# Performance work log

Hardware: AMD Instinct MI355X
Metric: run time of the kernel (lower is better)

Reference implementation:

```python
import jax, jax.numpy as jnp
import numpy as np

IN_FEATURES = 4096
OUT_FEATURES = 11008
BATCH = 16


def setup_inputs() -> dict:
    key = jax.random.key(0)
    k_x, k_w, k_s, k_b = jax.random.split(key, 4)
    x = jax.random.normal(k_x, (BATCH, IN_FEATURES), dtype=jnp.float32)
    # symmetric int8 weights stored as int32 for jax portability (values in [-127, 127])
    weight_int8 = jax.random.randint(k_w, (OUT_FEATURES, IN_FEATURES), -127, 128, dtype=jnp.int32)
    # per-output-channel scales, small positive values typical of int8 quantization
    weight_scale = jax.random.uniform(k_s, (OUT_FEATURES,), dtype=jnp.float32, minval=0.005, maxval=0.02)
    bias = jax.random.normal(k_b, (OUT_FEATURES,), dtype=jnp.float32)
    return {"x": x, "weight_int8": weight_int8, "weight_scale": weight_scale, "bias": bias}


def reference(x, weight_int8, weight_scale, bias):
    # Dequantize: w_dq[o, i] = int8[o, i] * scale[o]  -> fp32 [OUT, IN]
    w_dq = weight_int8.astype(x.dtype) * weight_scale[:, None]
    # F.linear: y = x @ w_dq.T + bias  -> [BATCH, OUT]
    return jnp.einsum("bi,oi->bo", x, w_dq) + bias
```

## Files before the change

### kernel.cpp

```cpp
#include <hip/hip_runtime.h>

#define IN_F   4096
#define OUT_F  11008
#define BATCH  16
#define BLOCK  256
#define SPLITK 8
#define KCHUNK (IN_F / SPLITK)
#define XPAD   8
#define XSTRIDE (KCHUNK + XPAD)
#define NSTEP  (KCHUNK / 32)

typedef short s16x8 __attribute__((ext_vector_type(8)));
typedef float f32x4 __attribute__((ext_vector_type(4)));
typedef int   i32x4 __attribute__((ext_vector_type(4)));

__global__ __launch_bounds__(BLOCK) void init_out_kernel(
    const float* __restrict__ bias, float* __restrict__ out)
{
    int idx = blockIdx.x * BLOCK + threadIdx.x;
    if (idx < BATCH * OUT_F) {
        int o = idx % OUT_F;
        out[idx] = bias[o];
    }
}

__device__ __forceinline__ unsigned short bf16_trunc_bits(float f) {
    return (unsigned short)(__float_as_uint(f) >> 16);
}

__global__ __launch_bounds__(BLOCK) void qlin_kernel(
    const float* __restrict__ x,
    const int*   __restrict__ w,
    const float* __restrict__ scale,
    float* __restrict__ out)
{
    __shared__ alignas(16) unsigned short xhi[BATCH * XSTRIDE];
    __shared__ alignas(16) unsigned short xlo[BATCH * XSTRIDE];

    const int tid  = threadIdx.x;
    const int lane = tid & 63;
    const int wv   = tid >> 6;
    const int n    = lane & 15;
    const int quad = lane >> 4;
    const int o0   = blockIdx.x * 64 + wv * 16;
    const int kb   = blockIdx.y * KCHUNK;

    const float4* __restrict__ xg = (const float4*)x;
    #pragma unroll
    for (int j = 0; j < (BATCH * KCHUNK / 4) / BLOCK; ++j) {
        int f  = tid + j * BLOCK;
        int b  = f >> 7;
        int kc = f & 127;
        float4 v = xg[(size_t)b * (IN_F / 4) + (kb >> 2) + kc];
        ushort4 h, l;
        {
            unsigned u;
            u = __float_as_uint(v.x); h.x = u >> 16;
            l.x = bf16_trunc_bits(v.x - __uint_as_float(u & 0xFFFF0000u));
            u = __float_as_uint(v.y); h.y = u >> 16;
            l.y = bf16_trunc_bits(v.y - __uint_as_float(u & 0xFFFF0000u));
            u = __float_as_uint(v.z); h.z = u >> 16;
            l.z = bf16_trunc_bits(v.z - __uint_as_float(u & 0xFFFF0000u));
            u = __float_as_uint(v.w); h.w = u >> 16;
            l.w = bf16_trunc_bits(v.w - __uint_as_float(u & 0xFFFF0000u));
        }
        *(ushort4*)&xhi[b * XSTRIDE + kc * 4] = h;
        *(ushort4*)&xlo[b * XSTRIDE + kc * 4] = l;
    }
    __syncthreads();

    const int* __restrict__ wrow = w + (size_t)(o0 + n) * IN_F + kb + quad * 8;
    i32x4 wa[2], wb[2];
    wa[0] = *(const i32x4*)(wrow);
    wb[0] = *(const i32x4*)(wrow + 4);

    f32x4 acc = {0.f, 0.f, 0.f, 0.f};

    #pragma unroll
    for (int s = 0; s < NSTEP; ++s) {
        const int cur = s & 1, nxt = cur ^ 1;
        if (s + 1 < NSTEP) {
            wa[nxt] = *(const i32x4*)(wrow + (s + 1) * 32);
            wb[nxt] = *(const i32x4*)(wrow + (s + 1) * 32 + 4);
        }

        s16x8 bfrag;
        #pragma unroll
        for (int e = 0; e < 4; ++e) {
            bfrag[e]     = (short)bf16_trunc_bits((float)wa[cur][e]);
            bfrag[4 + e] = (short)bf16_trunc_bits((float)wb[cur][e]);
        }

        const int xoff = n * XSTRIDE + s * 32 + quad * 8;
        s16x8 ah = *(const s16x8*)&xhi[xoff];
        s16x8 al = *(const s16x8*)&xlo[xoff];

        acc = __builtin_amdgcn_mfma_f32_16x16x32_bf16(ah, bfrag, acc, 0, 0, 0);
        acc = __builtin_amdgcn_mfma_f32_16x16x32_bf16(al, bfrag, acc, 0, 0, 0);
    }

    const int   o  = o0 + n;
    const float sc = scale[o];
    #pragma unroll
    for (int r = 0; r < 4; ++r) {
        const int b = quad * 4 + r;
        atomicAdd(&out[(size_t)b * OUT_F + o], acc[r] * sc);
    }
}

extern "C" void kernel_launch(void* const* d_in, const int* in_sizes, int n_in,
                              void* d_out, int out_size, void* d_ws, size_t ws_size,
                              hipStream_t stream) {
    const float* x     = (const float*)d_in[0];
    const int*   w     = (const int*)d_in[1];
    const float* scale = (const float*)d_in[2];
    const float* bias  = (const float*)d_in[3];
    float* out = (float*)d_out;

    init_out_kernel<<<(BATCH * OUT_F + BLOCK - 1) / BLOCK, BLOCK, 0, stream>>>(bias, out);

    dim3 grid(OUT_F / 64, SPLITK);
    qlin_kernel<<<grid, dim3(BLOCK), 0, stream>>>(x, w, scale, out);
}
```

Measured before the change: 261.8 us.

## Precompute bf16 hi/lo split of x in prep kernel, stream weights nontemporally

Moves the fp32-to-bf16 hi/lo splitting of x out of every qlin block and into a single prep kernel that also writes the bias init. The results go to workspace buffers. The main kernel now reads the x fragments straight from global memory with double-buffered prefetch, replacing the shared-memory staging and the __syncthreads barrier. Weight loads use nontemporal hints so the one-pass weight stream is less likely to evict x from cache. The x split also switches from truncation to round-to-nearest-even. The cost is one workspace round trip and x loads that now depend on L2/L1 hits instead of LDS.

```diff
diff --git a/kernel.cpp b/kernel.cpp
--- a/kernel.cpp
+++ b/kernel.cpp
@@ -6,37 +6,49 @@
 #define BLOCK  256
 #define SPLITK 8
 #define KCHUNK (IN_F / SPLITK)
-#define XPAD   8
-#define XSTRIDE (KCHUNK + XPAD)
 #define NSTEP  (KCHUNK / 32)
 
 typedef short s16x8 __attribute__((ext_vector_type(8)));
 typedef float f32x4 __attribute__((ext_vector_type(4)));
 typedef int   i32x4 __attribute__((ext_vector_type(4)));
+typedef unsigned short u16;
 
-__global__ __launch_bounds__(BLOCK) void init_out_kernel(
-    const float* __restrict__ bias, float* __restrict__ out)
+__device__ __forceinline__ u16 f32_to_bf16_rne(float f) {
+    unsigned u = __float_as_uint(f);
+    unsigned r = u + 0x7FFFu + ((u >> 16) & 1u);
+    return (u16)(r >> 16);
+}
+__device__ __forceinline__ float bf16_bits_to_f32(u16 h) {
+    return __uint_as_float((unsigned)h << 16);
+}
+
+__global__ __launch_bounds__(BLOCK) void prep_kernel(
+    const float* __restrict__ x, const float* __restrict__ bias,
+    float* __restrict__ out, u16* __restrict__ xhi, u16* __restrict__ xlo)
 {
-    int idx = blockIdx.x * BLOCK + threadIdx.x;
-    if (idx < BATCH * OUT_F) {
-        int o = idx % OUT_F;
-        out[idx] = bias[o];
+    const int bid = blockIdx.x;
+    const int tid = threadIdx.x;
+    if (bid < (BATCH * IN_F) / BLOCK) {
+        int i = bid * BLOCK + tid;
+        float v  = x[i];
+        u16 h    = f32_to_bf16_rne(v);
+        float hf = bf16_bits_to_f32(h);
+        u16 l    = f32_to_bf16_rne(v - hf);
+        xhi[i] = h;
+        xlo[i] = l;
+    } else {
+        int i = (bid - (BATCH * IN_F) / BLOCK) * BLOCK + tid;
+        out[i] = bias[i % OUT_F];
     }
 }
 
-__device__ __forceinline__ unsigned short bf16_trunc_bits(float f) {
-    return (unsigned short)(__float_as_uint(f) >> 16);
-}
-
 __global__ __launch_bounds__(BLOCK) void qlin_kernel(
-    const float* __restrict__ x,
     const int*   __restrict__ w,
     const float* __restrict__ scale,
+    const u16*   __restrict__ xhi,
+    const u16*   __restrict__ xlo,
     float* __restrict__ out)
 {
-    __shared__ alignas(16) unsigned short xhi[BATCH * XSTRIDE];
-    __shared__ alignas(16) unsigned short xlo[BATCH * XSTRIDE];
-
     const int tid  = threadIdx.x;
     const int lane = tid & 63;
     const int wv   = tid >> 6;
@@ -45,34 +57,16 @@
     const int o0   = blockIdx.x * 64 + wv * 16;
     const int kb   = blockIdx.y * KCHUNK;
 
-    const float4* __restrict__ xg = (const float4*)x;
-    #pragma unroll
-    for (int j = 0; j < (BATCH * KCHUNK / 4) / BLOCK; ++j) {
-        int f  = tid + j * BLOCK;
-        int b  = f >> 7;
-        int kc = f & 127;
-        float4 v = xg[(size_t)b * (IN_F / 4) + (kb >> 2) + kc];
-        ushort4 h, l;
-        {
-            unsigned u;
-            u = __float_as_uint(v.x); h.x = u >> 16;
-            l.x = bf16_trunc_bits(v.x - __uint_as_float(u & 0xFFFF0000u));
-            u = __float_as_uint(v.y); h.y = u >> 16;
-            l.y = bf16_trunc_bits(v.y - __uint_as_float(u & 0xFFFF0000u));
-            u = __float_as_uint(v.z); h.z = u >> 16;
-            l.z = bf16_trunc_bits(v.z - __uint_as_float(u & 0xFFFF0000u));
-            u = __float_as_uint(v.w); h.w = u >> 16;
-            l.w = bf16_trunc_bits(v.w - __uint_as_float(u & 0xFFFF0000u));
-        }
-        *(ushort4*)&xhi[b * XSTRIDE + kc * 4] = h;
-        *(ushort4*)&xlo[b * XSTRIDE + kc * 4] = l;
-    }
-    __syncthreads();
+    const int* __restrict__ wrow = w   + (size_t)(o0 + n) * IN_F + kb + quad * 8;
+    const u16* __restrict__ xh   = xhi + n * IN_F + kb + quad * 8;
+    const u16* __restrict__ xl   = xlo + n * IN_F + kb + quad * 8;
 
-    const int* __restrict__ wrow = w + (size_t)(o0 + n) * IN_F + kb + quad * 8;
     i32x4 wa[2], wb[2];
-    wa[0] = *(const i32x4*)(wrow);
-    wb[0] = *(const i32x4*)(wrow + 4);
+    s16x8 ah[2], al[2];
+    wa[0] = __builtin_nontemporal_load((const i32x4*)wrow);
+    wb[0] = __builtin_nontemporal_load((const i32x4*)(wrow + 4));
+    ah[0] = *(const s16x8*)xh;
+    al[0] = *(const s16x8*)xl;
 
     f32x4 acc = {0.f, 0.f, 0.f, 0.f};
 
@@ -80,23 +74,21 @@
     for (int s = 0; s < NSTEP; ++s) {
         const int cur = s & 1, nxt = cur ^ 1;
         if (s + 1 < NSTEP) {
-            wa[nxt] = *(const i32x4*)(wrow + (s + 1) * 32);
-            wb[nxt] = *(const i32x4*)(wrow + (s + 1) * 32 + 4);
+            wa[nxt] = __builtin_nontemporal_load((const i32x4*)(wrow + (s + 1) * 32));
+            wb[nxt] = __builtin_nontemporal_load((const i32x4*)(wrow + (s + 1) * 32 + 4));
+            ah[nxt] = *(const s16x8*)(xh + (s + 1) * 32);
+            al[nxt] = *(const s16x8*)(xl + (s + 1) * 32);
         }
 
         s16x8 bfrag;
         #pragma unroll
         for (int e = 0; e < 4; ++e) {
-            bfrag[e]     = (short)bf16_trunc_bits((float)wa[cur][e]);
-            bfrag[4 + e] = (short)bf16_trunc_bits((float)wb[cur][e]);
+            bfrag[e]     = (short)(u16)(__float_as_uint((float)wa[cur][e]) >> 16);
+            bfrag[4 + e] = (short)(u16)(__float_as_uint((float)wb[cur][e]) >> 16);
         }
 
-        const int xoff = n * XSTRIDE + s * 32 + quad * 8;
-        s16x8 ah = *(const s16x8*)&xhi[xoff];
-        s16x8 al = *(const s16x8*)&xlo[xoff];
-
-        acc = __builtin_amdgcn_mfma_f32_16x16x32_bf16(ah, bfrag, acc, 0, 0, 0);
-        acc = __builtin_amdgcn_mfma_f32_16x16x32_bf16(al, bfrag, acc, 0, 0, 0);
+        acc = __builtin_amdgcn_mfma_f32_16x16x32_bf16(ah[cur], bfrag, acc, 0, 0, 0);
+        acc = __builtin_amdgcn_mfma_f32_16x16x32_bf16(al[cur], bfrag, acc, 0, 0, 0);
     }
 
     const int   o  = o0 + n;
@@ -117,8 +109,12 @@
     const float* bias  = (const float*)d_in[3];
     float* out = (float*)d_out;
 
-    init_out_kernel<<<(BATCH * OUT_F + BLOCK - 1) / BLOCK, BLOCK, 0, stream>>>(bias, out);
+    u16* xhi = (u16*)d_ws;
+    u16* xlo = (u16*)((char*)d_ws + BATCH * IN_F * sizeof(u16));
+
+    prep_kernel<<<(BATCH * IN_F) / BLOCK + (BATCH * OUT_F) / BLOCK, BLOCK, 0, stream>>>(
+        x, bias, out, xhi, xlo);
 
     dim3 grid(OUT_F / 64, SPLITK);
-    qlin_kernel<<<grid, dim3(BLOCK), 0, stream>>>(x, w, scale, out);
+    qlin_kernel<<<grid, dim3(BLOCK), 0, stream>>>(w, scale, xhi, xlo, out);
 }
```

Result: no change. 266.3 us (+1.7%).
